# Optimization experiments

Measured on AMD Instinct MI355X. Metric: run time of the kernel, lower is better.

Reference implementation:

```python
import jax, jax.numpy as jnp
import numpy as np

NEG_SLOPE = 0.2

def setup_inputs() -> dict:
    key = jax.random.key(0)
    ks = jax.random.split(key, 10)
    N, E, L, D, H = 100000, 3200000, 200000, 128, 128
    x = jax.random.normal(ks[0], (N, D), dtype=jnp.float32)
    edge_index = jax.random.randint(ks[1], (2, E), 0, N, dtype=jnp.int64)
    edge_label_index = jax.random.randint(ks[2], (2, L), 0, N, dtype=jnp.int64)
    s = 1.0 / np.sqrt(D)
    W1l = jax.random.uniform(ks[3], (D, H), minval=-s, maxval=s, dtype=jnp.float32)
    b1 = jax.random.uniform(ks[4], (H,), minval=-s, maxval=s, dtype=jnp.float32)
    W1r = jax.random.uniform(ks[5], (D, H), minval=-s, maxval=s, dtype=jnp.float32)
    s2 = 1.0 / np.sqrt(H)
    W2l = jax.random.uniform(ks[6], (H, H), minval=-s2, maxval=s2, dtype=jnp.float32)
    b2 = jax.random.uniform(ks[7], (H,), minval=-s2, maxval=s2, dtype=jnp.float32)
    W2r = jax.random.uniform(ks[8], (H, H), minval=-s2, maxval=s2, dtype=jnp.float32)
    return {"x": x, "edge_index": edge_index, "edge_label_index": edge_label_index,
            "W1l": W1l, "b1": b1, "W1r": W1r, "W2l": W2l, "b2": b2, "W2r": W2r}

def reference(x, edge_index, edge_label_index, W1l, b1, W1r, W2l, b2, W2r):
    N = x.shape[0]
    src, dst = edge_index[0], edge_index[1]
    # in-degree for mean aggregation (clamped to avoid div-by-zero, matching mean over empty = 0)
    deg = jax.ops.segment_sum(jnp.ones_like(dst, dtype=x.dtype), dst, num_segments=N)
    inv_deg = (1.0 / jnp.maximum(deg, 1.0))[:, None]

    def sage(h, Wl, b, Wr):
        # mean of source-node features over incoming edges at each target node
        agg = jax.ops.segment_sum(h[src], dst, num_segments=N) * inv_deg
        return agg @ Wl + b + h @ Wr

    h = sage(x, W1l, b1, W1r)
    h = jnp.where(h >= 0, h, NEG_SLOPE * h)  # leaky_relu; eval mode so no dropout
    h = sage(h, W2l, b2, W2r)
    x_src = h[edge_label_index[0]]
    x_trg = h[edge_label_index[1]]
    return jnp.sum(x_src * x_trg, axis=1)
```

## Files before the change

### kernel.cpp

```cpp
#include <hip/hip_runtime.h>
#include <hip/hip_fp16.h>


#define D128 128
#define BSHIFT 9
#define BNODES 512

typedef __bf16 bf16x8 __attribute__((ext_vector_type(8)));
typedef float  f32x4  __attribute__((ext_vector_type(4)));
typedef _Float16 h2   __attribute__((ext_vector_type(2)));

union uh2cast { unsigned u; h2 h; };
__device__ inline h2 uash2(unsigned u) { uh2cast c; c.u = u; return c.h; }

__device__ inline unsigned short f2bf(float f) {
    unsigned u = __float_as_uint(f);
    u = u + 0x7FFF + ((u >> 16) & 1);
    return (unsigned short)(u >> 16);
}
__device__ inline float bf2f(unsigned short s) {
    return __uint_as_float(((unsigned)s) << 16);
}
__device__ inline unsigned packbf2(float lo, float hi) {
    return (unsigned)f2bf(lo) | ((unsigned)f2bf(hi) << 16);
}
__device__ inline unsigned char f2e5(float f) {
#if __has_builtin(__builtin_amdgcn_cvt_pk_bf8_f32)
    return (unsigned char)(__builtin_amdgcn_cvt_pk_bf8_f32(f, f, 0, false) & 0xFF);
#else
    unsigned short h = __half_as_ushort(__float2half(f));
    h = (unsigned short)(h + 0x7F + ((h >> 8) & 1));
    return (unsigned char)(h >> 8);
#endif
}


__global__ void prep_kernel(const float* __restrict__ in, unsigned short* __restrict__ outb,
                            unsigned char* __restrict__ out8, int n4,
                            const float* __restrict__ W1l, const float* __restrict__ W1r,
                            const float* __restrict__ W2l, const float* __restrict__ W2r,
                            unsigned short* __restrict__ packed,
                            const int* __restrict__ dst, int* __restrict__ bh,
                            int E, int castBlocks, int histBlocks) {
    int bid = blockIdx.x;
    int t = threadIdx.x;
    if (bid < castBlocks) {
        int i = bid * 256 + t;
        if (i >= n4) return;
        float4 v = ((const float4*)in)[i];
        ushort4 ob;
        ob.x = f2bf(v.x); ob.y = f2bf(v.y); ob.z = f2bf(v.z); ob.w = f2bf(v.w);
        ((ushort4*)outb)[i] = ob;
        unsigned p = (unsigned)f2e5(v.x) | ((unsigned)f2e5(v.y) << 8) |
                     ((unsigned)f2e5(v.z) << 16) | ((unsigned)f2e5(v.w) << 24);
        ((unsigned*)out8)[i] = p;
    } else if (bid < castBlocks + 256) {
        int tid = (bid - castBlocks) * 256 + t;
        int layer = tid >> 15;
        int r = tid & 32767;
        int j    = r & 7;
        int lane = (r >> 3) & 63;
        int nt   = (r >> 9) & 7;
        int kc   = (r >> 12) & 7;
        int k   = kc * 32 + ((lane >> 4) << 3) + j;
        int col = nt * 16 + (lane & 15);
        const float* Wl = layer ? W2l : W1l;
        const float* Wr = layer ? W2r : W1r;
        float v = (k < 128) ? Wl[k * 128 + col] : Wr[(k - 128) * 128 + col];
        packed[tid] = f2bf(v);
    } else {
        __shared__ int h[256];
        int hb = bid - castBlocks - 256;
        if (hb >= histBlocks) return;
        h[t] = 0;
        __syncthreads();
        int base = hb * 8192;
#pragma unroll
        for (int k = 0; k < 32; ++k) {
            int e = base + k * 256 + t;
            if (e < E) atomicAdd(&h[dst[e] >> BSHIFT], 1);
        }
        __syncthreads();
        bh[hb * 256 + t] = h[t];
    }
}


__global__ void bucket_scan(const int* __restrict__ bh, int nhb,
                            int* __restrict__ bucket_base, int* __restrict__ bucket_cur,
                            int* __restrict__ rowptr, int NB, int N, int E) {
    __shared__ int sc[256];
    __shared__ int orig[256];
    int t = threadIdx.x;
    int a0 = 0, a1 = 0, a2 = 0, a3 = 0, a4 = 0, a5 = 0, a6 = 0, a7 = 0;
    int b = 0;
    for (; b + 8 <= nhb; b += 8) {
        a0 += bh[(b + 0) * 256 + t];
        a1 += bh[(b + 1) * 256 + t];
        a2 += bh[(b + 2) * 256 + t];
        a3 += bh[(b + 3) * 256 + t];
        a4 += bh[(b + 4) * 256 + t];
        a5 += bh[(b + 5) * 256 + t];
        a6 += bh[(b + 6) * 256 + t];
        a7 += bh[(b + 7) * 256 + t];
    }
    for (; b < nhb; ++b) a0 += bh[b * 256 + t];
    int v = ((a0 + a1) + (a2 + a3)) + ((a4 + a5) + (a6 + a7));
    if (t >= NB) v = 0;
    orig[t] = v;
    sc[t] = v;
    __syncthreads();
    for (int off = 1; off < 256; off <<= 1) {
        int a = (t >= off) ? sc[t - off] : 0;
        __syncthreads();
        sc[t] += a;
        __syncthreads();
    }
    int ex = sc[t] - orig[t];
    if (t < NB) { bucket_base[t] = ex; bucket_cur[t] = ex; }
    if (t == 0) { bucket_base[NB] = E; rowptr[N] = E; }
}

__global__ void scatter_kernel(const int* __restrict__ src, const int* __restrict__ dst,
                               int* __restrict__ bucket_cur, int* __restrict__ pairs,
                               int E, int NB) {
    __shared__ int hist[256], lscan[256], gbase[256];
    __shared__ int lsrc[1024], ldst[1024];
    int t = threadIdx.x;
    hist[t] = 0;
    __syncthreads();
    int base = blockIdx.x * 1024;
    int total = E - base; if (total > 1024) total = 1024;

    int ms[4], md[4], mb[4], mr[4];
#pragma unroll
    for (int k = 0; k < 4; ++k) {
        int i = k * 256 + t;
        int e = base + i;
        mb[k] = -1;
        if (i < total) {
            ms[k] = src[e];
            md[k] = dst[e];
            mb[k] = md[k] >> BSHIFT;
            mr[k] = atomicAdd(&hist[mb[k]], 1);
        }
    }
    __syncthreads();
    lscan[t] = hist[t];
    __syncthreads();
    for (int off = 1; off < 256; off <<= 1) {
        int a = (t >= off) ? lscan[t - off] : 0;
        __syncthreads();
        lscan[t] += a;
        __syncthreads();
    }
    lscan[t] -= hist[t];
    if (t < NB && hist[t] > 0) gbase[t] = atomicAdd(&bucket_cur[t], hist[t]);
    __syncthreads();
#pragma unroll
    for (int k = 0; k < 4; ++k) {
        if (mb[k] >= 0) {
            int idx = lscan[mb[k]] + mr[k];
            lsrc[idx] = ms[k];
            ldst[idx] = md[k];
        }
    }
    __syncthreads();
#pragma unroll
    for (int k = 0; k < 4; ++k) {
        int i = k * 256 + t;
        if (i < total) {
            int d = ldst[i];
            int b = d >> BSHIFT;
            int pos = gbase[b] + (i - lscan[b]);
            pairs[pos] = (lsrc[i] << BSHIFT) | (d & (BNODES - 1));
        }
    }
}

__global__ void bucket_fill(const int* __restrict__ pairs, const int* __restrict__ bucket_base,
                            int* __restrict__ rowptr, int* __restrict__ srcs, int N) {
    __shared__ int hist[BNODES], excl[BNODES], sc[BNODES];
    int b = blockIdx.x;
    int t = threadIdx.x;
    int node0 = b << BSHIFT;
    int pbeg = bucket_base[b];
    int pend = bucket_base[b + 1];
    hist[t] = 0;
    __syncthreads();
    for (int p = pbeg + t; p < pend; p += BNODES) {
        atomicAdd(&hist[pairs[p] & (BNODES - 1)], 1);
    }
    __syncthreads();
    sc[t] = hist[t];
    __syncthreads();
    for (int off = 1; off < BNODES; off <<= 1) {
        int a = (t >= off) ? sc[t - off] : 0;
        __syncthreads();
        sc[t] += a;
        __syncthreads();
    }
    excl[t] = sc[t] - hist[t];
    int node = node0 + t;
    if (node < N) rowptr[node] = pbeg + excl[t];
    __syncthreads();
    hist[t] = 0;
    __syncthreads();
    for (int p = pbeg + t; p < pend; p += BNODES) {
        int w = pairs[p];
        int dl = w & (BNODES - 1);
        int c = atomicAdd(&hist[dl], 1);
        srcs[pbeg + excl[dl] + c] = (int)(((unsigned)w) >> BSHIFT) << 4;
    }
}


__device__ inline void pkacc8(h2* A, uint2 v) {
    A[0] += uash2((v.x << 8) & 0xFF00FF00u);
    A[1] += uash2(v.x & 0xFF00FF00u);
    A[2] += uash2((v.y << 8) & 0xFF00FF00u);
    A[3] += uash2(v.y & 0xFF00FF00u);
}

template <bool LEAKY>
__global__ void aggmm_kernel(const int* __restrict__ rowptr, const int* __restrict__ srcs,
                             const unsigned char* __restrict__ feat8,
                             const unsigned short* __restrict__ F,
                             const unsigned short* __restrict__ Wp,
                             const float* __restrict__ bias,
                             unsigned short* __restrict__ out,
                             unsigned char* __restrict__ out8, int N) {
    __shared__ unsigned short ldsA[4 * 16 * D128];
    int wid = threadIdx.x >> 6;
    int lane = threadIdx.x & 63;
    int q  = lane >> 4;
    int ql = lane & 15;
    int m0 = (blockIdx.x * 4 + wid) * 16;
    const uint2* f = (const uint2*)feat8;

    for (int r = 0; r < 16; ++r) {
        int n = m0 + r;
        if (n >= N) break;
        int beg = rowptr[n];
        int end = rowptr[n + 1];

        h2 A0[4], A1[4], A2[4], A3[4];
        h2 z; z[0] = (_Float16)0.f; z[1] = (_Float16)0.f;
#pragma unroll
        for (int k = 0; k < 4; ++k) { A0[k] = z; A1[k] = z; A2[k] = z; A3[k] = z; }

        int j = beg;
        for (; j + 16 <= end; j += 16) {
            int e0 = srcs[j + q];
            int e1 = srcs[j + 4 + q];
            int e2 = srcs[j + 8 + q];
            int e3 = srcs[j + 12 + q];
            uint2 v0 = f[e0 + ql];
            uint2 v1 = f[e1 + ql];
            uint2 v2 = f[e2 + ql];
            uint2 v3 = f[e3 + ql];
            pkacc8(A0, v0);
            pkacc8(A1, v1);
            pkacc8(A2, v2);
            pkacc8(A3, v3);
        }
        for (; j + 4 <= end; j += 4) {
            uint2 v = f[srcs[j + q] + ql];
            pkacc8(A0, v);
        }
        int rem = end - j;
        if (q < rem) {
            uint2 v = f[srcs[j + q] + ql];
            pkacc8(A1, v);
        }

        float c[8];
#pragma unroll
        for (int p = 0; p < 4; ++p) {
            float lo = (float)A0[p][0] + (float)A1[p][0] + (float)A2[p][0] + (float)A3[p][0];
            float hi = (float)A0[p][1] + (float)A1[p][1] + (float)A2[p][1] + (float)A3[p][1];
            int base = (p >> 1) * 4 + (p & 1);
            c[base] = lo;
            c[base + 2] = hi;
        }
#pragma unroll
        for (int k = 0; k < 8; ++k) {
            c[k] += __shfl_xor(c[k], 16, 64);
            c[k] += __shfl_xor(c[k], 32, 64);
        }
        int deg = end - beg;
        float inv = deg > 0 ? 1.0f / (float)deg : 0.f;
        if (q == 0) {
            uint4 rr;
            rr.x = packbf2(c[0] * inv, c[1] * inv);
            rr.y = packbf2(c[2] * inv, c[3] * inv);
            rr.z = packbf2(c[4] * inv, c[5] * inv);
            rr.w = packbf2(c[6] * inv, c[7] * inv);
            ((uint4*)ldsA)[wid * 256 + r * 16 + ql] = rr;
        }
    }
    __syncthreads();

    int rl = lane & 15;
    int rowF = m0 + rl;
    if (rowF > N - 1) rowF = N - 1;
    const unsigned short* ldsW = ldsA + wid * 16 * D128;

    f32x4 acc[8];
#pragma unroll
    for (int nt = 0; nt < 8; ++nt) acc[nt] = (f32x4){0.f, 0.f, 0.f, 0.f};

#pragma unroll
    for (int kc = 0; kc < 8; ++kc) {
        bf16x8 af;
        if (kc < 4) af = *(const bf16x8*)(ldsW + rl * D128 + kc * 32 + q * 8);
        else        af = *(const bf16x8*)(F + (size_t)rowF * D128 + (kc - 4) * 32 + q * 8);
        const unsigned short* wp = Wp + ((size_t)kc * 8) * 512 + lane * 8;
#pragma unroll
        for (int nt = 0; nt < 8; ++nt) {
            bf16x8 bf = *(const bf16x8*)(wp + nt * 512);
            acc[nt] = __builtin_amdgcn_mfma_f32_16x16x32_bf16(af, bf, acc[nt], 0, 0, 0);
        }
    }

#pragma unroll
    for (int nt = 0; nt < 8; ++nt) {
        int col = nt * 16 + rl;
        float bv = bias[col];
#pragma unroll
        for (int r = 0; r < 4; ++r) {
            int row = m0 + q * 4 + r;
            if (row < N) {
                float v = acc[nt][r] + bv;
                if (LEAKY) v = v >= 0.f ? v : 0.2f * v;
                out[(size_t)row * D128 + col] = f2bf(v);
                if (out8) out8[(size_t)row * D128 + col] = f2e5(v);
            }
        }
    }
}


__global__ void score_kernel(const int* __restrict__ eli, const unsigned short* __restrict__ h,
                             float* __restrict__ out, int L) {
    int wave = threadIdx.x >> 6;
    int lane = threadIdx.x & 63;
    int l0 = (blockIdx.x * 4 + wave) * 4;
    if (l0 >= L) return;
    const ushort2* h2p = (const ushort2*)h;
    int a[4], b[4];
#pragma unroll
    for (int k = 0; k < 4; ++k) {
        int l = l0 + k;
        if (l > L - 1) l = L - 1;
        a[k] = eli[l];
        b[k] = eli[L + l];
    }
    float p[4];
#pragma unroll
    for (int k = 0; k < 4; ++k) {
        ushort2 u = h2p[(size_t)a[k] * 64 + lane];
        ushort2 v = h2p[(size_t)b[k] * 64 + lane];
        p[k] = bf2f(u.x) * bf2f(v.x) + bf2f(u.y) * bf2f(v.y);
    }
#pragma unroll
    for (int off = 32; off > 0; off >>= 1) {
#pragma unroll
        for (int k = 0; k < 4; ++k) p[k] += __shfl_down(p[k], off, 64);
    }
    if (lane == 0) {
#pragma unroll
        for (int k = 0; k < 4; ++k) {
            if (l0 + k < L) out[l0 + k] = p[k];
        }
    }
}


extern "C" void kernel_launch(void* const* d_in, const int* in_sizes, int n_in,
                              void* d_out, int out_size, void* d_ws, size_t ws_size,
                              hipStream_t stream) {
    const float* x   = (const float*)d_in[0];
    const int*   ei  = (const int*)d_in[1];
    const int*   eli = (const int*)d_in[2];
    const float* W1l = (const float*)d_in[3];
    const float* b1  = (const float*)d_in[4];
    const float* W1r = (const float*)d_in[5];
    const float* W2l = (const float*)d_in[6];
    const float* b2  = (const float*)d_in[7];
    const float* W2r = (const float*)d_in[8];

    const int N = in_sizes[0] / D128;
    const int E = in_sizes[1] / 2;
    const int L = in_sizes[2] / 2;
    const int* srcp = ei;
    const int* dstp = ei + E;
    const int NB = (N + BNODES - 1) >> BSHIFT;

    char* ws = (char*)d_ws;
    size_t off = 0;
    auto alloc = [&](size_t bytes) -> void* {
        void* p = ws + off;
        off += (bytes + 255) & ~(size_t)255;
        return p;
    };
    const int histBlocks = (E + 8191) / 8192;
    int*   rowptr = (int*)alloc((size_t)(N + 1) * sizeof(int));
    int*   bh     = (int*)alloc((size_t)histBlocks * 256 * sizeof(int));
    int*   bbase  = (int*)alloc(257 * sizeof(int));
    int*   bcur   = (int*)alloc(256 * sizeof(int));
    int*   pairs  = (int*)alloc((size_t)E * sizeof(int));
    int*   srcs   = (int*)alloc(((size_t)E + 16) * sizeof(int));
    unsigned short* xb   = (unsigned short*)alloc((size_t)N * D128 * 2);
    unsigned char*  x8   = (unsigned char*)alloc((size_t)N * D128);
    unsigned char*  h1f8 = (unsigned char*)alloc((size_t)N * D128);
    unsigned short* h1b  = (unsigned short*)alloc((size_t)N * D128 * 2);
    unsigned short* h2b  = (unsigned short*)alloc((size_t)N * D128 * 2);
    unsigned short* Wp   = (unsigned short*)alloc(2 * 32768 * 2);
    (void)ws_size; (void)n_in; (void)out_size;

    int n4 = N * D128 / 4;
    int castBlocks = (n4 + 255) / 256;
    prep_kernel<<<castBlocks + 256 + histBlocks, 256, 0, stream>>>(
        x, xb, x8, n4, W1l, W1r, W2l, W2r, Wp, dstp, bh, E, castBlocks, histBlocks);

    bucket_scan<<<1, 256, 0, stream>>>(bh, histBlocks, bbase, bcur, rowptr, NB, N, E);
    scatter_kernel<<<(E + 1023) / 1024, 256, 0, stream>>>(srcp, dstp, bcur, pairs, E, NB);
    bucket_fill<<<NB, BNODES, 0, stream>>>(pairs, bbase, rowptr, srcs, N);

    int mmBlocks = (N + 63) / 64;
    aggmm_kernel<true><<<mmBlocks, 256, 0, stream>>>(rowptr, srcs, x8, xb, Wp, b1,
                                                     h1b, h1f8, N);

    aggmm_kernel<false><<<mmBlocks, 256, 0, stream>>>(rowptr, srcs, h1f8, h1b, Wp + 32768,
                                                      b2, h2b, (unsigned char*)nullptr, N);

    score_kernel<<<(L + 15) / 16, 256, 0, stream>>>(eli, h2b, (float*)d_out, L);
}
```

Baseline: 454.5 us.

## Split aggregation rows and output columns across waves in 16-row blocks

```diff
diff --git a/kernel.cpp b/kernel.cpp
--- a/kernel.cpp
+++ b/kernel.cpp
@@ -12,6 +12,8 @@
 
 union uh2cast { unsigned u; h2 h; };
 __device__ inline h2 uash2(unsigned u) { uh2cast c; c.u = u; return c.h; }
+union u4bf8cast { uint4 u; bf16x8 b; };
+__device__ inline bf16x8 u4asbf8(uint4 u) { u4bf8cast c; c.u = u; return c.b; }
 
 __device__ inline unsigned short f2bf(float f) {
     unsigned u = __float_as_uint(f);
@@ -230,73 +232,76 @@
                              const float* __restrict__ bias,
                              unsigned short* __restrict__ out,
                              unsigned char* __restrict__ out8, int N) {
-    __shared__ unsigned short ldsA[4 * 16 * D128];
+    __shared__ unsigned short ldsA[16 * D128];
     int wid = threadIdx.x >> 6;
     int lane = threadIdx.x & 63;
     int q  = lane >> 4;
     int ql = lane & 15;
-    int m0 = (blockIdx.x * 4 + wid) * 16;
+    int m0 = blockIdx.x * 16;
     const uint2* f = (const uint2*)feat8;
 
-    for (int r = 0; r < 16; ++r) {
-        int n = m0 + r;
-        if (n >= N) break;
-        int beg = rowptr[n];
-        int end = rowptr[n + 1];
-
-        h2 A0[4], A1[4], A2[4], A3[4];
-        h2 z; z[0] = (_Float16)0.f; z[1] = (_Float16)0.f;
-#pragma unroll
-        for (int k = 0; k < 4; ++k) { A0[k] = z; A1[k] = z; A2[k] = z; A3[k] = z; }
-
-        int j = beg;
-        for (; j + 16 <= end; j += 16) {
-            int e0 = srcs[j + q];
-            int e1 = srcs[j + 4 + q];
-            int e2 = srcs[j + 8 + q];
-            int e3 = srcs[j + 12 + q];
-            uint2 v0 = f[e0 + ql];
-            uint2 v1 = f[e1 + ql];
-            uint2 v2 = f[e2 + ql];
-            uint2 v3 = f[e3 + ql];
-            pkacc8(A0, v0);
-            pkacc8(A1, v1);
-            pkacc8(A2, v2);
-            pkacc8(A3, v3);
-        }
-        for (; j + 4 <= end; j += 4) {
-            uint2 v = f[srcs[j + q] + ql];
-            pkacc8(A0, v);
-        }
-        int rem = end - j;
-        if (q < rem) {
-            uint2 v = f[srcs[j + q] + ql];
-            pkacc8(A1, v);
-        }
-
-        float c[8];
-#pragma unroll
-        for (int p = 0; p < 4; ++p) {
-            float lo = (float)A0[p][0] + (float)A1[p][0] + (float)A2[p][0] + (float)A3[p][0];
-            float hi = (float)A0[p][1] + (float)A1[p][1] + (float)A2[p][1] + (float)A3[p][1];
-            int base = (p >> 1) * 4 + (p & 1);
-            c[base] = lo;
-            c[base + 2] = hi;
-        }
-#pragma unroll
-        for (int k = 0; k < 8; ++k) {
-            c[k] += __shfl_xor(c[k], 16, 64);
-            c[k] += __shfl_xor(c[k], 32, 64);
-        }
-        int deg = end - beg;
-        float inv = deg > 0 ? 1.0f / (float)deg : 0.f;
-        if (q == 0) {
-            uint4 rr;
-            rr.x = packbf2(c[0] * inv, c[1] * inv);
-            rr.y = packbf2(c[2] * inv, c[3] * inv);
-            rr.z = packbf2(c[4] * inv, c[5] * inv);
-            rr.w = packbf2(c[6] * inv, c[7] * inv);
-            ((uint4*)ldsA)[wid * 256 + r * 16 + ql] = rr;
+#pragma unroll
+    for (int i = 0; i < 4; ++i) {
+        int rloc = wid * 4 + i;
+        int n = m0 + rloc;
+        if (n < N) {
+            int beg = rowptr[n];
+            int end = rowptr[n + 1];
+
+            h2 A0[4], A1[4], A2[4], A3[4];
+            h2 z; z[0] = (_Float16)0.f; z[1] = (_Float16)0.f;
+#pragma unroll
+            for (int k = 0; k < 4; ++k) { A0[k] = z; A1[k] = z; A2[k] = z; A3[k] = z; }
+
+            int j = beg;
+            for (; j + 16 <= end; j += 16) {
+                int e0 = srcs[j + q];
+                int e1 = srcs[j + 4 + q];
+                int e2 = srcs[j + 8 + q];
+                int e3 = srcs[j + 12 + q];
+                uint2 v0 = f[e0 + ql];
+                uint2 v1 = f[e1 + ql];
+                uint2 v2 = f[e2 + ql];
+                uint2 v3 = f[e3 + ql];
+                pkacc8(A0, v0);
+                pkacc8(A1, v1);
+                pkacc8(A2, v2);
+                pkacc8(A3, v3);
+            }
+            for (; j + 4 <= end; j += 4) {
+                uint2 v = f[srcs[j + q] + ql];
+                pkacc8(A0, v);
+            }
+            int rem = end - j;
+            if (q < rem) {
+                uint2 v = f[srcs[j + q] + ql];
+                pkacc8(A1, v);
+            }
+
+            float c[8];
+#pragma unroll
+            for (int p = 0; p < 4; ++p) {
+                float lo = (float)A0[p][0] + (float)A1[p][0] + (float)A2[p][0] + (float)A3[p][0];
+                float hi = (float)A0[p][1] + (float)A1[p][1] + (float)A2[p][1] + (float)A3[p][1];
+                int base = (p >> 1) * 4 + (p & 1);
+                c[base] = lo;
+                c[base + 2] = hi;
+            }
+#pragma unroll
+            for (int k = 0; k < 8; ++k) {
+                c[k] += __shfl_xor(c[k], 16, 64);
+                c[k] += __shfl_xor(c[k], 32, 64);
+            }
+            int deg = end - beg;
+            float inv = deg > 0 ? 1.0f / (float)deg : 0.f;
+            if (q == 0) {
+                uint4 rr;
+                rr.x = packbf2(c[0] * inv, c[1] * inv);
+                rr.y = packbf2(c[2] * inv, c[3] * inv);
+                rr.z = packbf2(c[4] * inv, c[5] * inv);
+                rr.w = packbf2(c[6] * inv, c[7] * inv);
+                ((uint4*)ldsA)[rloc * 16 + ((ql + rloc) & 15)] = rr;
+            }
         }
     }
     __syncthreads();
@@ -304,34 +309,37 @@
     int rl = lane & 15;
     int rowF = m0 + rl;
     if (rowF > N - 1) rowF = N - 1;
-    const unsigned short* ldsW = ldsA + wid * 16 * D128;
-
-    f32x4 acc[8];
-#pragma unroll
-    for (int nt = 0; nt < 8; ++nt) acc[nt] = (f32x4){0.f, 0.f, 0.f, 0.f};
+    int nt0 = wid * 2;
+
+    f32x4 acc[2];
+    acc[0] = (f32x4){0.f, 0.f, 0.f, 0.f};
+    acc[1] = (f32x4){0.f, 0.f, 0.f, 0.f};
 
 #pragma unroll
     for (int kc = 0; kc < 8; ++kc) {
         bf16x8 af;
-        if (kc < 4) af = *(const bf16x8*)(ldsW + rl * D128 + kc * 32 + q * 8);
-        else        af = *(const bf16x8*)(F + (size_t)rowF * D128 + (kc - 4) * 32 + q * 8);
+        if (kc < 4) {
+            uint4 u = ((const uint4*)ldsA)[rl * 16 + ((kc * 4 + q + rl) & 15)];
+            af = u4asbf8(u);
+        } else {
+            af = *(const bf16x8*)(F + (size_t)rowF * D128 + (kc - 4) * 32 + q * 8);
+        }
         const unsigned short* wp = Wp + ((size_t)kc * 8) * 512 + lane * 8;
-#pragma unroll
-        for (int nt = 0; nt < 8; ++nt) {
-            bf16x8 bf = *(const bf16x8*)(wp + nt * 512);
-            acc[nt] = __builtin_amdgcn_mfma_f32_16x16x32_bf16(af, bf, acc[nt], 0, 0, 0);
-        }
-    }
-
-#pragma unroll
-    for (int nt = 0; nt < 8; ++nt) {
-        int col = nt * 16 + rl;
+        bf16x8 bf0 = *(const bf16x8*)(wp + nt0 * 512);
+        bf16x8 bf1 = *(const bf16x8*)(wp + (nt0 + 1) * 512);
+        acc[0] = __builtin_amdgcn_mfma_f32_16x16x32_bf16(af, bf0, acc[0], 0, 0, 0);
+        acc[1] = __builtin_amdgcn_mfma_f32_16x16x32_bf16(af, bf1, acc[1], 0, 0, 0);
+    }
+
+#pragma unroll
+    for (int t = 0; t < 2; ++t) {
+        int col = (nt0 + t) * 16 + rl;
         float bv = bias[col];
 #pragma unroll
         for (int r = 0; r < 4; ++r) {
             int row = m0 + q * 4 + r;
             if (row < N) {
-                float v = acc[nt][r] + bv;
+                float v = acc[t][r] + bv;
                 if (LEAKY) v = v >= 0.f ? v : 0.2f * v;
                 out[(size_t)row * D128 + col] = f2bf(v);
                 if (out8) out8[(size_t)row * D128 + col] = f2e5(v);
@@ -428,7 +436,7 @@
     scatter_kernel<<<(E + 1023) / 1024, 256, 0, stream>>>(srcp, dstp, bcur, pairs, E, NB);
     bucket_fill<<<NB, BNODES, 0, stream>>>(pairs, bbase, rowptr, srcs, N);
 
-    int mmBlocks = (N + 63) / 64;
+    int mmBlocks = (N + 15) / 16;
     aggmm_kernel<true><<<mmBlocks, 256, 0, stream>>>(rowptr, srcs, x8, xb, Wp, b1,
                                                      h1b, h1f8, N);
 
```

Result: faster. 445.1 us (-2.1%).
